# Kernel tuning notes

Hardware: AMD Instinct MI355X
Metric: run time of the kernel (lower is better)

Reference implementation:

```python
import jax, jax.numpy as jnp
import numpy as np

N_SIGMA = 2
N_CLASS = 8
FG_WEIGHT = jnp.array([10., 10., 10., 40., 80., 100., 60., 20.], dtype=jnp.float32)
W_INST, W_VAR, W_SEED = 1.0, 10.0, 1.0
MIN_PIXELS = 128


def lovasz_hinge_flat(logits, labels):
    # logits, labels: [P] flat; labels in {0,1}
    signs = 2.0 * labels - 1.0
    errors = 1.0 - logits * signs
    order = jnp.argsort(-errors)  # descending
    errors_sorted = errors[order]
    gt_sorted = labels[order]
    gts = gt_sorted.sum()
    inter = gts - jnp.cumsum(gt_sorted)
    union = gts + jnp.cumsum(1.0 - gt_sorted)
    jac = 1.0 - inter / union
    grad = jnp.concatenate([jac[:1], jac[1:] - jac[:-1]])
    return jnp.dot(jax.nn.relu(errors_sorted), jax.lax.stop_gradient(grad))


def setup_inputs() -> dict:
    key = jax.random.key(0)
    k1, k2, k3, k4 = jax.random.split(key, 4)
    B, H, W, N = 2, 512, 1024, 8
    prediction = jax.random.normal(k1, (B, 12, H, W), dtype=jnp.float32)
    bbox = jax.random.randint(k2, (B, 9, H, W), 0, 2, dtype=jnp.int32)
    masks = jax.random.randint(k3, (B, N, H, W), 0, 2, dtype=jnp.int32)
    cls_ids = jax.random.randint(k4, (B, N), 0, 8, dtype=jnp.int32)
    return {"prediction": prediction, "bbox": bbox, "masks": masks, "cls_ids": cls_ids}


def _forward(prediction, bbox, masks, cls_ids):
    B, C, H, W = prediction.shape
    N = masks.shape[1]
    sg = jax.lax.stop_gradient
    # coordinate map: full 2048/1024 linspace sliced to [:W]/[:H], as in the buffer
    xm = jnp.linspace(0.0, 2.0, 2048, dtype=prediction.dtype)[:W]
    ym = jnp.linspace(0.0, 1.0, 1024, dtype=prediction.dtype)[:H]
    xym = jnp.stack([jnp.broadcast_to(xm[None, :], (H, W)),
                     jnp.broadcast_to(ym[:, None], (H, W))], axis=0)  # [2,H,W]

    spatial_emb = jnp.tanh(prediction[:, 0:2]) + xym[None]            # [B,2,H,W]
    sigma = prediction[:, 2:2 + N_SIGMA]                               # [B,2,H,W]
    seed = jax.nn.sigmoid(prediction[:, 2 + N_SIGMA:2 + N_SIGMA + N_CLASS])  # [B,8,H,W]

    # background seed loss: sum over cls 1..8 of seed[cls-1]^2 where bbox[cls]==0
    bg = bbox[:, 1:9] == 0                                             # [B,8,H,W]
    seed_bg = jnp.sum(jnp.where(bg, seed * seed, 0.0), axis=(1, 2, 3))  # [B]

    m = (masks > 0).astype(prediction.dtype)                           # [B,N,H,W]
    cnt = m.sum(axis=(2, 3))                                           # [B,N]
    valid = (cnt >= MIN_PIXELS).astype(prediction.dtype)               # [B,N]
    cnt_safe = jnp.maximum(cnt, 1.0)

    # per-instance masked means (to_center=False -> center from spatial_emb)
    center = jnp.einsum('bnhw,bchw->bnc', m, spatial_emb) / cnt_safe[..., None]  # [B,N,2]
    s_mean = jnp.einsum('bnhw,bchw->bnc', m, sigma) / cnt_safe[..., None]        # [B,N,2]

    # var loss: mean over [n_sigma, P] of (sigma_in - s.detach())^2
    diff2 = (sigma[:, None] - sg(s_mean)[..., None, None]) ** 2        # [B,N,2,H,W]
    var_inst = jnp.einsum('bnchw,bnhw->bn', diff2, m) / (N_SIGMA * cnt_safe)

    s_exp = jnp.exp(s_mean * 10.0)                                     # [B,N,2]
    d2 = (spatial_emb[:, None] - center[..., None, None]) ** 2         # [B,N,2,H,W]
    dist = jnp.exp(-jnp.einsum('bnchw,bnc->bnhw', d2, s_exp))          # [B,N,H,W]

    # lovasz hinge per instance on dist*2-1 vs mask
    logits = (dist * 2.0 - 1.0).reshape(B * N, H * W)
    labels = m.reshape(B * N, H * W)
    lov = jax.vmap(lovasz_hinge_flat)(logits, labels).reshape(B, N)    # [B,N]

    # foreground seed loss
    seed_cls = jnp.take_along_axis(seed, cls_ids[..., None, None].astype(jnp.int32), axis=1)  # [B,N,H,W]
    fw = FG_WEIGHT[cls_ids]                                            # [B,N]
    seed_fg = fw * jnp.einsum('bnhw,bnhw->bn', m, (seed_cls - sg(dist)) ** 2)

    obj = valid.sum(axis=1)                                            # [B]
    obj_safe = jnp.maximum(obj, 1.0)
    inst_l = jnp.sum(lov * valid, axis=1) / obj_safe
    var_l = jnp.sum(var_inst * valid, axis=1) / obj_safe
    seed_l = (seed_bg + jnp.sum(seed_fg * valid, axis=1)) / (H * W)
    loss = jnp.mean(W_INST * inst_l + W_VAR * var_l + W_SEED * seed_l)
    return loss


def reference(prediction, bbox, masks, cls_ids):
    return _forward(prediction, bbox, masks, cls_ids)
```

## Files before the change

kernel.cpp:

```cpp
#include <hip/hip_runtime.h>
#include <cstdint>
#include <cstddef>

#define HW 524288
#define NBIN 2048


__device__ __forceinline__ float wred(float v) {
#pragma unroll
  for (int o = 32; o > 0; o >>= 1) v += __shfl_xor(v, o, 64);
  return v;
}

__device__ __forceinline__ float fsig(float x) {
  return __builtin_amdgcn_rcpf(1.f + expf(-x));
}

__global__ __launch_bounds__(256) void pass1(
    const float* __restrict__ pred, const int* __restrict__ bbox,
    const int* __restrict__ masks, double* __restrict__ acc,
    double* __restrict__ seedbg)
{
  const int b = blockIdx.y;
  const int tid = threadIdx.x;
  const int chunk = blockIdx.x;
  const float* pb = pred + (size_t)b * 12 * HW;
  const int*   mk = masks + (size_t)b * 8 * HW;
  const int*   bb = bbox  + (size_t)b * 9 * HW + HW;

  float c[8] = {0}, cx[8] = {0}, cy[8] = {0}, sx[8] = {0}, sy[8] = {0},
        sxx[8] = {0}, syy[8] = {0};
  float sbg = 0.f;

#pragma unroll
  for (int k = 0; k < 8; k++) {
    int idx = chunk * 2048 + k * 256 + tid;
    int h = idx >> 10, w = idx & 1023;
    float p0 = pb[idx], p1 = pb[HW + idx];
    float ex = tanhf(p0) + (float)(w * (2.0 / 2047.0));
    float ey = tanhf(p1) + (float)(h * (1.0 / 1023.0));
    float s0 = pb[2 * HW + idx], s1 = pb[3 * HW + idx];
#pragma unroll
    for (int n = 0; n < 8; n++) {
      float mf = (mk[n * HW + idx] > 0) ? 1.f : 0.f;
      c[n] += mf; cx[n] += mf * ex; cy[n] += mf * ey;
      sx[n] += mf * s0; sy[n] += mf * s1;
      sxx[n] += mf * s0 * s0; syy[n] += mf * s1 * s1;
    }
#pragma unroll
    for (int cc = 0; cc < 8; cc++) {
      float sv = pb[(4 + cc) * HW + idx];
      int bv = bb[cc * HW + idx];
      float sg = fsig(sv);
      sbg += (bv == 0) ? sg * sg : 0.f;
    }
  }

  __shared__ float red[4][57];
  int lane = tid & 63, wid = tid >> 6;
#pragma unroll
  for (int n = 0; n < 8; n++) {
    float r0 = wred(c[n]),  r1 = wred(cx[n]), r2 = wred(cy[n]),
          r3 = wred(sx[n]), r4 = wred(sy[n]), r5 = wred(sxx[n]),
          r6 = wred(syy[n]);
    if (lane == 0) {
      red[wid][n * 7 + 0] = r0; red[wid][n * 7 + 1] = r1;
      red[wid][n * 7 + 2] = r2; red[wid][n * 7 + 3] = r3;
      red[wid][n * 7 + 4] = r4; red[wid][n * 7 + 5] = r5;
      red[wid][n * 7 + 6] = r6;
    }
  }
  { float r = wred(sbg); if (lane == 0) red[wid][56] = r; }
  __syncthreads();
  if (tid < 57) {
    float s = red[0][tid] + red[1][tid] + red[2][tid] + red[3][tid];
    if (tid < 56) {
      int n = tid / 7, q = tid % 7;
      atomicAdd(&acc[((size_t)b * 8 + n) * 8 + q], (double)s);
    } else {
      atomicAdd(&seedbg[b], (double)s);
    }
  }
}

__global__ __launch_bounds__(1024) void pass3(
    const float* __restrict__ pred, const int* __restrict__ masks,
    const int* __restrict__ cls_ids, double* __restrict__ acc,
    unsigned* __restrict__ ghist)
{
  const int seg = blockIdx.y;
  const int b = seg >> 3, n = seg & 7;
  const int tid = threadIdx.x;
  __shared__ unsigned hist[NBIN * 2];
  __shared__ float red[16];
  for (int j = tid; j < NBIN * 2; j += 1024) hist[j] = 0;

  const double* a = acc + seg * 8;
  double cntd = a[0];
  double cs = cntd < 1.0 ? 1.0 : cntd;
  float cxv = (float)(a[1] / cs), cyv = (float)(a[2] / cs);
  float sex = expf((float)(a[3] / cs) * 10.f);
  float sey = expf((float)(a[4] / cs) * 10.f);
  int cls = cls_ids[b * 8 + n];
  const float* pb = pred + (size_t)b * 12 * HW;
  const float* seedp = pb + (size_t)(4 + cls) * HW;
  const int* mp = masks + (size_t)seg * HW;
  __syncthreads();

  float sf = 0.f;
  int base = blockIdx.x * 32768;
#pragma unroll 4
  for (int i = 0; i < 32; i++) {
    int idx = base + i * 1024 + tid;
    float p0 = pb[idx], p1 = pb[HW + idx];
    int m = (mp[idx] > 0) ? 1 : 0;
    float sv = seedp[idx];
    int h = idx >> 10, w = idx & 1023;
    float ex = tanhf(p0) + (float)(w * (2.0 / 2047.0));
    float ey = tanhf(p1) + (float)(h * (1.0 / 1023.0));
    float dx = ex - cxv, dy = ey - cyv;
    float d = expf(-(dx * dx * sex + dy * dy * sey));
    float sg = fsig(sv);
    float df = sg - d;
    sf += m ? df * df : 0.f;
    float e = m ? 2.f - 2.f * d : 2.f * d;
    int k = (int)(e * 1024.f); k = k > (NBIN - 1) ? (NBIN - 1) : k;
    atomicAdd(&hist[k * 2 + m], 1u);
  }
  __syncthreads();

  unsigned* gh = ghist + (size_t)seg * NBIN * 2;
  for (int j = tid; j < NBIN * 2; j += 1024) {
    unsigned v = hist[j];
    if (v) atomicAdd(&gh[j], v);
  }

  float r = wred(sf);
  int lane = tid & 63, wid = tid >> 6;
  if (lane == 0) red[wid] = r;
  __syncthreads();
  if (tid == 0) {
    float t = 0.f;
    for (int w2 = 0; w2 < 16; w2++) t += red[w2];
    atomicAdd(&acc[seg * 8 + 7], (double)t);
  }
}

__global__ __launch_bounds__(64) void pass4(
    const unsigned* __restrict__ ghist, const double* __restrict__ acc,
    float* __restrict__ lov)
{
  int seg = blockIdx.x;
  int lane = threadIdx.x;
  const unsigned* gh = ghist + (size_t)seg * NBIN * 2;
  double G = acc[seg * 8 + 0];

  unsigned cntT = 0, posT = 0;
#pragma unroll
  for (int i = 0; i < 32; i++) {
    int kk = (NBIN - 1) - lane * 32 - i;
    unsigned h1 = gh[kk * 2 + 1], h0 = gh[kk * 2 + 0];
    cntT += h1 + h0; posT += h1;
  }
  unsigned ic = cntT, ip = posT;
  for (int o = 1; o < 64; o <<= 1) {
    unsigned yc = __shfl_up(ic, o, 64), yp = __shfl_up(ip, o, 64);
    if (lane >= o) { ic += yc; ip += yp; }
  }
  unsigned p = ic - cntT, C = ip - posT;

  double S = 0.0;
  for (int i = 0; i < 32; i++) {
    int kk = (NBIN - 1) - lane * 32 - i;
    unsigned n1 = gh[kk * 2 + 1], n0 = gh[kk * 2 + 0];
    double ec = (kk + 0.5) * (1.0 / 1024.0);
    if (n1) {
      S += (double)n1 * ec / (G + (double)(p - C));
      p += n1; C += n1;
    }
    if (n0) {
      double rem = G - (double)C;
      if (rem > 0.0) {
        double aa = rem + (double)(p - C) + (double)C - (double)C + (double)p - (double)p;
        aa = G + (double)(p - C);
        S += ec * rem * (1.0 / aa - 1.0 / (aa + (double)n0));
      }
      p += n0;
    }
  }
#pragma unroll
  for (int o = 32; o > 0; o >>= 1) S += __shfl_xor(S, o, 64);
  if (lane == 0) lov[seg] = (float)S;
}

__global__ void pass5(const double* __restrict__ acc,
                      const double* __restrict__ seedbg,
                      const float* __restrict__ lov,
                      const int* __restrict__ cls_ids,
                      float* __restrict__ out)
{
  __shared__ double lval[16], vval[16], sval[16];
  __shared__ float valv[16];
  int t = threadIdx.x;
  const float FG[8] = {10.f, 10.f, 10.f, 40.f, 80.f, 100.f, 60.f, 20.f};
  if (t < 16) {
    const double* a = acc + t * 8;
    double cnt = a[0];
    double cs = cnt < 1.0 ? 1.0 : cnt;
    double smx = a[3] / cs, smy = a[4] / cs;
    double var = ((a[5] - cnt * smx * smx) + (a[6] - cnt * smy * smy)) / (2.0 * cs);
    lval[t] = (double)lov[t];
    vval[t] = var;
    sval[t] = (double)FG[cls_ids[t]] * a[7];
    valv[t] = (cnt >= 128.0) ? 1.f : 0.f;
  }
  __syncthreads();
  if (t == 0) {
    double total = 0.0;
    for (int b = 0; b < 2; b++) {
      double obj = 0, inst = 0, varl = 0, sfg = 0;
      for (int n = 0; n < 8; n++) {
        int s = b * 8 + n;
        double v = (double)valv[s];
        obj += v; inst += lval[s] * v; varl += vval[s] * v; sfg += sval[s] * v;
      }
      double objs = obj < 1.0 ? 1.0 : obj;
      double seedl = (seedbg[b] + sfg) / (double)HW;
      total += inst / objs + 10.0 * (varl / objs) + seedl;
    }
    out[0] = (float)(0.5 * total);
  }
}

extern "C" void kernel_launch(void* const* d_in, const int* in_sizes, int n_in,
                              void* d_out, int out_size, void* d_ws, size_t ws_size,
                              hipStream_t stream)
{
  (void)in_sizes; (void)n_in; (void)out_size; (void)ws_size;
  const float* pred  = (const float*)d_in[0];
  const int*   bbox  = (const int*)d_in[1];
  const int*   masks = (const int*)d_in[2];
  const int*   cls   = (const int*)d_in[3];

  char* ws = (char*)d_ws;
  double*   acc    = (double*)(ws + 0);
  double*   seedbg = (double*)(ws + 1024);
  float*    lov    = (float*)(ws + 1040);
  unsigned* ghist  = (unsigned*)(ws + 4096);

  hipMemsetAsync(d_ws, 0, 266240, stream);
  pass1<<<dim3(256, 2), 256, 0, stream>>>(pred, bbox, masks, acc, seedbg);
  pass3<<<dim3(16, 16), 1024, 0, stream>>>(pred, masks, cls, acc, ghist);
  pass4<<<16, 64, 0, stream>>>(ghist, acc, lov);
  pass5<<<1, 64, 0, stream>>>(acc, seedbg, lov, cls, (float*)d_out);
}
```

Before: 205.1 us.

## Vectorize pass1/pass3 loads to 128-bit and fuse final reduction kernels

Pass1 and pass3 now read predictions, masks and bbox as float4/int4, with each thread handling four consecutive pixels. This cuts the number of load instructions and should make better use of memory bandwidth. The lovasz histogram scan and the final loss combination move into one 1024-thread block, which removes one kernel launch and the lov round-trip through global memory. The risk is higher register pressure in pass1 from the unrolled per-pixel work.

```diff
diff --git a/kernel.cpp b/kernel.cpp
--- a/kernel.cpp
+++ b/kernel.cpp
@@ -3,6 +3,7 @@
 #include <cstddef>
 
 #define HW 524288
+#define HW4 (HW / 4)
 #define NBIN 2048
 
 
@@ -23,36 +24,54 @@
 {
   const int b = blockIdx.y;
   const int tid = threadIdx.x;
-  const int chunk = blockIdx.x;
-  const float* pb = pred + (size_t)b * 12 * HW;
-  const int*   mk = masks + (size_t)b * 8 * HW;
-  const int*   bb = bbox  + (size_t)b * 9 * HW + HW;
+  const float4* pb4 = (const float4*)(pred + (size_t)b * 12 * HW);
+  const int4*   mk4 = (const int4*)(masks + (size_t)b * 8 * HW);
+  const int4*   bb4 = (const int4*)(bbox  + (size_t)b * 9 * HW + HW);
 
   float c[8] = {0}, cx[8] = {0}, cy[8] = {0}, sx[8] = {0}, sy[8] = {0},
         sxx[8] = {0}, syy[8] = {0};
   float sbg = 0.f;
 
 #pragma unroll
-  for (int k = 0; k < 8; k++) {
-    int idx = chunk * 2048 + k * 256 + tid;
+  for (int k = 0; k < 2; k++) {
+    int g = blockIdx.x * 512 + k * 256 + tid;
+    int idx = g << 2;
     int h = idx >> 10, w = idx & 1023;
-    float p0 = pb[idx], p1 = pb[HW + idx];
-    float ex = tanhf(p0) + (float)(w * (2.0 / 2047.0));
-    float ey = tanhf(p1) + (float)(h * (1.0 / 1023.0));
-    float s0 = pb[2 * HW + idx], s1 = pb[3 * HW + idx];
+    float4 p0 = pb4[g];
+    float4 p1 = pb4[HW4 + g];
+    float4 s0 = pb4[2 * HW4 + g];
+    float4 s1 = pb4[3 * HW4 + g];
+    float exv[4], eyv[4], s0v[4] = {s0.x, s0.y, s0.z, s0.w},
+                         s1v[4] = {s1.x, s1.y, s1.z, s1.w};
+    float p0v[4] = {p0.x, p0.y, p0.z, p0.w}, p1v[4] = {p1.x, p1.y, p1.z, p1.w};
+#pragma unroll
+    for (int j = 0; j < 4; j++) {
+      exv[j] = tanhf(p0v[j]) + (float)((w + j) * (2.0 / 2047.0));
+      eyv[j] = tanhf(p1v[j]) + (float)(h * (1.0 / 1023.0));
+    }
 #pragma unroll
     for (int n = 0; n < 8; n++) {
-      float mf = (mk[n * HW + idx] > 0) ? 1.f : 0.f;
-      c[n] += mf; cx[n] += mf * ex; cy[n] += mf * ey;
-      sx[n] += mf * s0; sy[n] += mf * s1;
-      sxx[n] += mf * s0 * s0; syy[n] += mf * s1 * s1;
+      int4 mv = mk4[n * HW4 + g];
+      int mvv[4] = {mv.x, mv.y, mv.z, mv.w};
+#pragma unroll
+      for (int j = 0; j < 4; j++) {
+        float mf = (mvv[j] > 0) ? 1.f : 0.f;
+        c[n] += mf; cx[n] += mf * exv[j]; cy[n] += mf * eyv[j];
+        sx[n] += mf * s0v[j]; sy[n] += mf * s1v[j];
+        sxx[n] += mf * s0v[j] * s0v[j]; syy[n] += mf * s1v[j] * s1v[j];
+      }
     }
 #pragma unroll
     for (int cc = 0; cc < 8; cc++) {
-      float sv = pb[(4 + cc) * HW + idx];
-      int bv = bb[cc * HW + idx];
-      float sg = fsig(sv);
-      sbg += (bv == 0) ? sg * sg : 0.f;
+      float4 sv = pb4[(4 + cc) * HW4 + g];
+      int4 bv = bb4[cc * HW4 + g];
+      float svv[4] = {sv.x, sv.y, sv.z, sv.w};
+      int bvv[4] = {bv.x, bv.y, bv.z, bv.w};
+#pragma unroll
+      for (int j = 0; j < 4; j++) {
+        float sg = fsig(svv[j]);
+        sbg += (bvv[j] == 0) ? sg * sg : 0.f;
+      }
     }
   }
 
@@ -102,30 +121,39 @@
   float sex = expf((float)(a[3] / cs) * 10.f);
   float sey = expf((float)(a[4] / cs) * 10.f);
   int cls = cls_ids[b * 8 + n];
-  const float* pb = pred + (size_t)b * 12 * HW;
-  const float* seedp = pb + (size_t)(4 + cls) * HW;
-  const int* mp = masks + (size_t)seg * HW;
+  const float4* pb4 = (const float4*)(pred + (size_t)b * 12 * HW);
+  const float4* sp4 = pb4 + (size_t)(4 + cls) * HW4;
+  const int4*   mp4 = (const int4*)(masks + (size_t)seg * HW);
   __syncthreads();
 
   float sf = 0.f;
-  int base = blockIdx.x * 32768;
-#pragma unroll 4
-  for (int i = 0; i < 32; i++) {
-    int idx = base + i * 1024 + tid;
-    float p0 = pb[idx], p1 = pb[HW + idx];
-    int m = (mp[idx] > 0) ? 1 : 0;
-    float sv = seedp[idx];
+  int gbase = blockIdx.x * 8192;
+#pragma unroll 2
+  for (int i = 0; i < 8; i++) {
+    int g = gbase + i * 1024 + tid;
+    int idx = g << 2;
     int h = idx >> 10, w = idx & 1023;
-    float ex = tanhf(p0) + (float)(w * (2.0 / 2047.0));
-    float ey = tanhf(p1) + (float)(h * (1.0 / 1023.0));
-    float dx = ex - cxv, dy = ey - cyv;
-    float d = expf(-(dx * dx * sex + dy * dy * sey));
-    float sg = fsig(sv);
-    float df = sg - d;
-    sf += m ? df * df : 0.f;
-    float e = m ? 2.f - 2.f * d : 2.f * d;
-    int k = (int)(e * 1024.f); k = k > (NBIN - 1) ? (NBIN - 1) : k;
-    atomicAdd(&hist[k * 2 + m], 1u);
+    float4 p0 = pb4[g];
+    float4 p1 = pb4[HW4 + g];
+    int4 mv = mp4[g];
+    float4 sv = sp4[g];
+    float p0v[4] = {p0.x, p0.y, p0.z, p0.w}, p1v[4] = {p1.x, p1.y, p1.z, p1.w};
+    float svv[4] = {sv.x, sv.y, sv.z, sv.w};
+    int mvv[4] = {mv.x, mv.y, mv.z, mv.w};
+#pragma unroll
+    for (int j = 0; j < 4; j++) {
+      int m = (mvv[j] > 0) ? 1 : 0;
+      float ex = tanhf(p0v[j]) + (float)((w + j) * (2.0 / 2047.0));
+      float ey = tanhf(p1v[j]) + (float)(h * (1.0 / 1023.0));
+      float dx = ex - cxv, dy = ey - cyv;
+      float d = expf(-(dx * dx * sex + dy * dy * sey));
+      float sg = fsig(svv[j]);
+      float df = sg - d;
+      sf += m ? df * df : 0.f;
+      float e = m ? 2.f - 2.f * d : 2.f * d;
+      int k = (int)(e * 1024.f); k = k > (NBIN - 1) ? (NBIN - 1) : k;
+      atomicAdd(&hist[k * 2 + m], 1u);
+    }
   }
   __syncthreads();
 
@@ -146,21 +174,23 @@
   }
 }
 
-__global__ __launch_bounds__(64) void pass4(
+__global__ __launch_bounds__(1024) void pass4(
     const unsigned* __restrict__ ghist, const double* __restrict__ acc,
-    float* __restrict__ lov)
-{
-  int seg = blockIdx.x;
-  int lane = threadIdx.x;
-  const unsigned* gh = ghist + (size_t)seg * NBIN * 2;
+    const double* __restrict__ seedbg, const int* __restrict__ cls_ids,
+    float* __restrict__ out)
+{
+  const int seg = threadIdx.x >> 6;
+  const int lane = threadIdx.x & 63;
+  __shared__ float lovs[16];
+  const uint2* gh2 = (const uint2*)(ghist + (size_t)seg * NBIN * 2);
   double G = acc[seg * 8 + 0];
 
   unsigned cntT = 0, posT = 0;
 #pragma unroll
   for (int i = 0; i < 32; i++) {
     int kk = (NBIN - 1) - lane * 32 - i;
-    unsigned h1 = gh[kk * 2 + 1], h0 = gh[kk * 2 + 0];
-    cntT += h1 + h0; posT += h1;
+    uint2 hh = gh2[kk];
+    cntT += hh.x + hh.y; posT += hh.y;
   }
   unsigned ic = cntT, ip = posT;
   for (int o = 1; o < 64; o <<= 1) {
@@ -172,7 +202,8 @@
   double S = 0.0;
   for (int i = 0; i < 32; i++) {
     int kk = (NBIN - 1) - lane * 32 - i;
-    unsigned n1 = gh[kk * 2 + 1], n0 = gh[kk * 2 + 0];
+    uint2 hh = gh2[kk];
+    unsigned n1 = hh.y, n0 = hh.x;
     double ec = (kk + 0.5) * (1.0 / 1024.0);
     if (n1) {
       S += (double)n1 * ec / (G + (double)(p - C));
@@ -181,8 +212,7 @@
     if (n0) {
       double rem = G - (double)C;
       if (rem > 0.0) {
-        double aa = rem + (double)(p - C) + (double)C - (double)C + (double)p - (double)p;
-        aa = G + (double)(p - C);
+        double aa = G + (double)(p - C);
         S += ec * rem * (1.0 / aa - 1.0 / (aa + (double)n0));
       }
       p += n0;
@@ -190,39 +220,27 @@
   }
 #pragma unroll
   for (int o = 32; o > 0; o >>= 1) S += __shfl_xor(S, o, 64);
-  if (lane == 0) lov[seg] = (float)S;
-}
-
-__global__ void pass5(const double* __restrict__ acc,
-                      const double* __restrict__ seedbg,
-                      const float* __restrict__ lov,
-                      const int* __restrict__ cls_ids,
-                      float* __restrict__ out)
-{
-  __shared__ double lval[16], vval[16], sval[16];
-  __shared__ float valv[16];
-  int t = threadIdx.x;
-  const float FG[8] = {10.f, 10.f, 10.f, 40.f, 80.f, 100.f, 60.f, 20.f};
-  if (t < 16) {
-    const double* a = acc + t * 8;
-    double cnt = a[0];
-    double cs = cnt < 1.0 ? 1.0 : cnt;
-    double smx = a[3] / cs, smy = a[4] / cs;
-    double var = ((a[5] - cnt * smx * smx) + (a[6] - cnt * smy * smy)) / (2.0 * cs);
-    lval[t] = (double)lov[t];
-    vval[t] = var;
-    sval[t] = (double)FG[cls_ids[t]] * a[7];
-    valv[t] = (cnt >= 128.0) ? 1.f : 0.f;
-  }
-  __syncthreads();
-  if (t == 0) {
+  if (lane == 0) lovs[seg] = (float)S;
+  __syncthreads();
+
+  if (threadIdx.x == 0) {
+    const float FG[8] = {10.f, 10.f, 10.f, 40.f, 80.f, 100.f, 60.f, 20.f};
     double total = 0.0;
     for (int b = 0; b < 2; b++) {
       double obj = 0, inst = 0, varl = 0, sfg = 0;
       for (int n = 0; n < 8; n++) {
         int s = b * 8 + n;
-        double v = (double)valv[s];
-        obj += v; inst += lval[s] * v; varl += vval[s] * v; sfg += sval[s] * v;
+        const double* a = acc + s * 8;
+        double cnt = a[0];
+        double cs = cnt < 1.0 ? 1.0 : cnt;
+        double smx = a[3] / cs, smy = a[4] / cs;
+        double var = ((a[5] - cnt * smx * smx) + (a[6] - cnt * smy * smy)) /
+                     (2.0 * cs);
+        double v = (cnt >= 128.0) ? 1.0 : 0.0;
+        obj += v;
+        inst += (double)lovs[s] * v;
+        varl += var * v;
+        sfg += (double)FG[cls_ids[s]] * a[7] * v;
       }
       double objs = obj < 1.0 ? 1.0 : obj;
       double seedl = (seedbg[b] + sfg) / (double)HW;
@@ -245,12 +263,10 @@
   char* ws = (char*)d_ws;
   double*   acc    = (double*)(ws + 0);
   double*   seedbg = (double*)(ws + 1024);
-  float*    lov    = (float*)(ws + 1040);
   unsigned* ghist  = (unsigned*)(ws + 4096);
 
   hipMemsetAsync(d_ws, 0, 266240, stream);
   pass1<<<dim3(256, 2), 256, 0, stream>>>(pred, bbox, masks, acc, seedbg);
   pass3<<<dim3(16, 16), 1024, 0, stream>>>(pred, masks, cls, acc, ghist);
-  pass4<<<16, 64, 0, stream>>>(ghist, acc, lov);
-  pass5<<<1, 64, 0, stream>>>(acc, seedbg, lov, cls, (float*)d_out);
-}
+  pass4<<<1, 1024, 0, stream>>>(ghist, acc, seedbg, cls, (float*)d_out);
+}
```

After: 218.0 us. +6.3%, slower.
